# Kernel optimization log

Hardware: AMD Instinct MI355X
Metric: run time of the kernel (lower is better)

## Reference

```python
import jax, jax.numpy as jnp
import numpy as np

B, S, H = 4096, 64, 512


def setup_inputs() -> dict:
    key = jax.random.key(0)
    ks = jax.random.split(key, 10)
    sc = 1.0 / np.sqrt(H)
    return {
        "facts": jax.random.normal(ks[0], (B, S, H), dtype=jnp.float32),
        "G": jax.random.uniform(ks[1], (B, S), dtype=jnp.float32),
        "Wr": jax.random.normal(ks[2], (H, H), dtype=jnp.float32) * sc,
        "br": jnp.zeros((H,), dtype=jnp.float32),
        "Ur": jax.random.normal(ks[3], (H, H), dtype=jnp.float32) * sc,
        "bur": jnp.zeros((H,), dtype=jnp.float32),
        "W": jax.random.normal(ks[4], (H, H), dtype=jnp.float32) * sc,
        "bw": jnp.zeros((H,), dtype=jnp.float32),
        "U": jax.random.normal(ks[5], (H, H), dtype=jnp.float32) * sc,
        "bu": jnp.zeros((H,), dtype=jnp.float32),
    }


def reference(facts, G, Wr, br, Ur, bur, W, bw, U, bu):
    # facts: (B, S, H), G: (B, S) -> output (B, H)
    # Precompute input projections for all steps (batched GEMMs, hoisted out of scan)
    fWr = jnp.einsum('bsh,oh->bso', facts, Wr) + br  # (B,S,H)
    fW = jnp.einsum('bsh,oh->bso', facts, W) + bw    # (B,S,H)

    def step(C, xs):
        fwr_t, fw_t, g_t = xs  # (B,H), (B,H), (B,)
        r = jax.nn.sigmoid(fwr_t + C @ Ur.T + bur)
        h_tilda = jnp.tanh(fw_t + r * (C @ U.T + bu))
        g = g_t[:, None]
        h = g * h_tilda + (1.0 - g) * C
        return h, None

    C0 = jnp.zeros((facts.shape[0], facts.shape[2]), dtype=facts.dtype)
    xs = (jnp.swapaxes(fWr, 0, 1), jnp.swapaxes(fW, 0, 1), G.T)  # time-major
    C, _ = jax.lax.scan(step, C0, xs)
    return C
```

## Files before the change

kernel.cpp:

```cpp
#include <hip/hip_runtime.h>

#define B_ 4096
#define S_ 64
#define H_ 512
#define BM 128
#define BN 64
#define BK 64
#define NIT (H_ / BK)

typedef _Float16 half8 __attribute__((ext_vector_type(8)));
typedef _Float16 half4 __attribute__((ext_vector_type(4)));
typedef float float4v __attribute__((ext_vector_type(4)));
typedef unsigned int uint4v __attribute__((ext_vector_type(4)));

__global__ void convert_weights_kernel(const float* __restrict__ Wr, const float* __restrict__ W,
                                       const float* __restrict__ Ur, const float* __restrict__ U,
                                       _Float16* __restrict__ out) {
    const float* src;
    switch (blockIdx.y) {
        case 0: src = Wr; break;
        case 1: src = W;  break;
        case 2: src = Ur; break;
        default: src = U; break;
    }
    int i = (blockIdx.x * blockDim.x + threadIdx.x) * 8;
    float4v a = *(const float4v*)(src + i);
    float4v b = *(const float4v*)(src + i + 4);
    half8 h;
    h[0] = (_Float16)a[0]; h[1] = (_Float16)a[1]; h[2] = (_Float16)a[2]; h[3] = (_Float16)a[3];
    h[4] = (_Float16)b[0]; h[5] = (_Float16)b[1]; h[6] = (_Float16)b[2]; h[7] = (_Float16)b[3];
    *(half8*)(out + (size_t)blockIdx.y * H_ * H_ + i) = h;
}

template<bool LAST>
__global__ __launch_bounds__(256, 1)
void gru_step_kernel(const float* __restrict__ facts, const float* __restrict__ G,
                     const _Float16* __restrict__ wf,
                     const float* __restrict__ br, const float* __restrict__ bur,
                     const float* __restrict__ bw, const float* __restrict__ bu,
                     const _Float16* __restrict__ c_in, _Float16* __restrict__ c_out,
                     float* __restrict__ out32, int t)
{
    extern __shared__ _Float16 sm[];
    const int tid = threadIdx.x;
    const int lane = tid & 63;
    const int wid = tid >> 6;
    const int l15 = lane & 15;
    const int l4  = lane >> 4;
    const int wm = wid >> 1;
    const int wn = wid & 1;
    const int b0 = blockIdx.x * BM;
    const int n0 = blockIdx.y * BN;

    float4v acc[4][4][2];
#pragma unroll
    for (int w = 0; w < 4; ++w)
#pragma unroll
        for (int m = 0; m < 4; ++m)
#pragma unroll
            for (int n = 0; n < 2; ++n)
                acc[w][m][n] = (float4v){0.f, 0.f, 0.f, 0.f};

    float4v sf[8];
    uint4v  scv[4];
    uint4v  swv[8];

    const int f_row = wid * 32 + l4;
    const int f_col = l15 * 4;
    const int c_row = wid * 32 + (lane >> 3);
    const int c_chk = lane & 7;
    const int w_row = lane >> 3;

    const float* fbase = facts + ((size_t)b0 * S_ + t) * H_;

    auto issue = [&](int kk) {
        const int k0 = kk * BK;
#pragma unroll
        for (int j = 0; j < 8; ++j)
            sf[j] = *(const float4v*)(fbase + (size_t)(f_row + j * 4) * (S_ * H_) + k0 + f_col);
#pragma unroll
        for (int j = 0; j < 4; ++j)
            scv[j] = *(const uint4v*)(c_in + (size_t)(b0 + c_row + j * 8) * H_ + k0 + c_chk * 8);
#pragma unroll
        for (int j = 0; j < 8; ++j)
            swv[j] = *(const uint4v*)(wf + (size_t)wid * (H_ * H_) + (size_t)(n0 + w_row + j * 8) * H_ + k0 + c_chk * 8);
    };

    auto stage = [&](int sel) {
        _Float16* bf  = sm + sel * 32768;
        _Float16* bc  = bf + 8192;
        _Float16* bwt = bf + 16384;
#pragma unroll
        for (int j = 0; j < 8; ++j) {
            int row = f_row + j * 4;
            half4 h;
            h[0] = (_Float16)sf[j][0]; h[1] = (_Float16)sf[j][1];
            h[2] = (_Float16)sf[j][2]; h[3] = (_Float16)sf[j][3];
            int c16 = (l15 >> 1) ^ (row & 7);
            *(half4*)&bf[row * 64 + c16 * 8 + (l15 & 1) * 4] = h;
        }
#pragma unroll
        for (int j = 0; j < 4; ++j) {
            int row = c_row + j * 8;
            *(uint4v*)&bc[row * 64 + ((c_chk ^ (row & 7)) << 3)] = scv[j];
        }
#pragma unroll
        for (int j = 0; j < 8; ++j) {
            int row = w_row + j * 8;
            *(uint4v*)&bwt[(wid * 64 + row) * 64 + ((c_chk ^ (row & 7)) << 3)] = swv[j];
        }
    };

    auto compute = [&](int sel) {
        const _Float16* bf  = sm + sel * 32768;
        const _Float16* bc  = bf + 8192;
        const _Float16* bwt = bf + 16384;
#pragma unroll
        for (int s = 0; s < 2; ++s) {
            half8 fa[4], fc[4], wb[4][2];
            const int kc = s * 4 + l4;
#pragma unroll
            for (int m = 0; m < 4; ++m) {
                int row = wm * 64 + m * 16 + l15;
                int off = row * 64 + ((kc ^ (row & 7)) << 3);
                fa[m] = *(const half8*)&bf[off];
                fc[m] = *(const half8*)&bc[off];
            }
#pragma unroll
            for (int w = 0; w < 4; ++w)
#pragma unroll
                for (int n = 0; n < 2; ++n) {
                    int row = wn * 32 + n * 16 + l15;
                    wb[w][n] = *(const half8*)&bwt[(w * 64 + row) * 64 + ((kc ^ (row & 7)) << 3)];
                }
#pragma unroll
            for (int m = 0; m < 4; ++m)
#pragma unroll
                for (int n = 0; n < 2; ++n) {
                    acc[0][m][n] = __builtin_amdgcn_mfma_f32_16x16x32_f16(fa[m], wb[0][n], acc[0][m][n], 0, 0, 0);
                    acc[1][m][n] = __builtin_amdgcn_mfma_f32_16x16x32_f16(fa[m], wb[1][n], acc[1][m][n], 0, 0, 0);
                    acc[2][m][n] = __builtin_amdgcn_mfma_f32_16x16x32_f16(fc[m], wb[2][n], acc[2][m][n], 0, 0, 0);
                    acc[3][m][n] = __builtin_amdgcn_mfma_f32_16x16x32_f16(fc[m], wb[3][n], acc[3][m][n], 0, 0, 0);
                }
        }
    };

    issue(0);
#pragma unroll
    for (int kk = 0; kk < NIT; ++kk) {
        stage(kk & 1);
        if (kk + 1 < NIT) issue(kk + 1);
        __syncthreads();
        compute(kk & 1);
    }

    const int col_base = n0 + wn * 32;
    const int row_base = b0 + wm * 64;
#pragma unroll
    for (int n = 0; n < 2; ++n) {
        const int col = col_base + n * 16 + l15;
        const float brv = br[col] + bur[col];
        const float bwv = bw[col];
        const float buv = bu[col];
#pragma unroll
        for (int m = 0; m < 4; ++m) {
#pragma unroll
            for (int r = 0; r < 4; ++r) {
                const int row = row_base + m * 16 + l4 * 4 + r;
                float apre = acc[0][m][n][r] + acc[2][m][n][r] + brv;
                float rg = 1.0f / (1.0f + __expf(-apre));
                float x = (acc[1][m][n][r] + bwv) + rg * (acc[3][m][n][r] + buv);
                float e2 = __expf(2.0f * x);
                float ht = 1.0f - 2.0f / (e2 + 1.0f);
                float g = G[(size_t)row * S_ + t];
                float cold = (float)c_in[(size_t)row * H_ + col];
                float h = g * ht + (1.0f - g) * cold;
                if (LAST) out32[(size_t)row * H_ + col] = h;
                else      c_out[(size_t)row * H_ + col] = (_Float16)h;
            }
        }
    }
}

extern "C" void kernel_launch(void* const* d_in, const int* in_sizes, int n_in,
                              void* d_out, int out_size, void* d_ws, size_t ws_size,
                              hipStream_t stream) {
    const float* facts = (const float*)d_in[0];
    const float* G     = (const float*)d_in[1];
    const float* Wr    = (const float*)d_in[2];
    const float* br    = (const float*)d_in[3];
    const float* Ur    = (const float*)d_in[4];
    const float* bur   = (const float*)d_in[5];
    const float* W     = (const float*)d_in[6];
    const float* bw    = (const float*)d_in[7];
    const float* U     = (const float*)d_in[8];
    const float* bu    = (const float*)d_in[9];

    _Float16* wf16 = (_Float16*)d_ws;
    _Float16* c0   = wf16 + 4 * H_ * H_;
    _Float16* c1   = c0 + (size_t)B_ * H_;

    hipMemsetAsync(c0, 0, (size_t)B_ * H_ * sizeof(_Float16), stream);
    convert_weights_kernel<<<dim3(H_ * H_ / (256 * 8), 4), 256, 0, stream>>>(Wr, W, Ur, U, wf16);

    dim3 grid(B_ / BM, H_ / BN);
    const size_t lds = 131072;
    _Float16* bufs[2] = {c0, c1};
    for (int t = 0; t < S_; ++t) {
        _Float16* cin  = bufs[t & 1];
        _Float16* cout = bufs[(t & 1) ^ 1];
        if (t == S_ - 1)
            gru_step_kernel<true><<<grid, 256, lds, stream>>>(facts, G, wf16, br, bur, bw, bu,
                                                              cin, cout, (float*)d_out, t);
        else
            gru_step_kernel<false><<<grid, 256, lds, stream>>>(facts, G, wf16, br, bur, bw, bu,
                                                               cin, cout, nullptr, t);
    }
}
```

Before: 1.922 ms.

## Hoist input projections into one batched GEMM, leaving only recurrent GEMMs per step

Splits the work into a single up-front GEMM that computes facts·[Wr;W]^T plus biases for all time steps into a time-major fp16 buffer P, and a slimmer per-step kernel that only multiplies the hidden state by Ur and U. The per-step kernel reads the precomputed projections from P in its epilogue. The step kernel also uses smaller tiles, less LDS and two blocks per CU for more occupancy. The cost is a large extra fp16 workspace buffer (S·B·1024 halves) plus its write and reread traffic, and an extra rounding of the projections to fp16.

```diff
diff --git a/kernel.cpp b/kernel.cpp
--- a/kernel.cpp
+++ b/kernel.cpp
@@ -3,10 +3,6 @@
 #define B_ 4096
 #define S_ 64
 #define H_ 512
-#define BM 128
-#define BN 64
-#define BK 64
-#define NIT (H_ / BK)
 
 typedef _Float16 half8 __attribute__((ext_vector_type(8)));
 typedef _Float16 half4 __attribute__((ext_vector_type(4)));
@@ -32,14 +28,10 @@
     *(half8*)(out + (size_t)blockIdx.y * H_ * H_ + i) = h;
 }
 
-template<bool LAST>
-__global__ __launch_bounds__(256, 1)
-void gru_step_kernel(const float* __restrict__ facts, const float* __restrict__ G,
-                     const _Float16* __restrict__ wf,
-                     const float* __restrict__ br, const float* __restrict__ bur,
-                     const float* __restrict__ bw, const float* __restrict__ bu,
-                     const _Float16* __restrict__ c_in, _Float16* __restrict__ c_out,
-                     float* __restrict__ out32, int t)
+__global__ __launch_bounds__(256, 2)
+void gemm_p_kernel(const float* __restrict__ facts, const _Float16* __restrict__ wAB,
+                   const float* __restrict__ br, const float* __restrict__ bur,
+                   const float* __restrict__ bw, _Float16* __restrict__ P)
 {
     extern __shared__ _Float16 sm[];
     const int tid = threadIdx.x;
@@ -47,49 +39,38 @@
     const int wid = tid >> 6;
     const int l15 = lane & 15;
     const int l4  = lane >> 4;
-    const int wm = wid >> 1;
-    const int wn = wid & 1;
-    const int b0 = blockIdx.x * BM;
-    const int n0 = blockIdx.y * BN;
-
-    float4v acc[4][4][2];
-#pragma unroll
-    for (int w = 0; w < 4; ++w)
-#pragma unroll
-        for (int m = 0; m < 4; ++m)
-#pragma unroll
-            for (int n = 0; n < 2; ++n)
-                acc[w][m][n] = (float4v){0.f, 0.f, 0.f, 0.f};
+    const int wm = wid >> 1, wn = wid & 1;
+    const int bid = blockIdx.x;
+    const int idx = bid & 63;
+    const int mt = (bid >> 6) * 8 + (idx & 7);
+    const int nt = idx >> 3;
+    const int m0 = mt * 128, n0 = nt * 128;
+
+    float4v acc[4][4];
+#pragma unroll
+    for (int m = 0; m < 4; ++m)
+#pragma unroll
+        for (int n = 0; n < 4; ++n) acc[m][n] = (float4v){0.f, 0.f, 0.f, 0.f};
 
     float4v sf[8];
-    uint4v  scv[4];
-    uint4v  swv[8];
-
+    uint4v  swv[4];
     const int f_row = wid * 32 + l4;
     const int f_col = l15 * 4;
-    const int c_row = wid * 32 + (lane >> 3);
-    const int c_chk = lane & 7;
-    const int w_row = lane >> 3;
-
-    const float* fbase = facts + ((size_t)b0 * S_ + t) * H_;
+    const int b_row = wid * 32 + (lane >> 3);
+    const int b_chk = lane & 7;
 
     auto issue = [&](int kk) {
-        const int k0 = kk * BK;
+        const int k0 = kk * 64;
 #pragma unroll
         for (int j = 0; j < 8; ++j)
-            sf[j] = *(const float4v*)(fbase + (size_t)(f_row + j * 4) * (S_ * H_) + k0 + f_col);
+            sf[j] = *(const float4v*)(facts + (size_t)(m0 + f_row + j * 4) * H_ + k0 + f_col);
 #pragma unroll
         for (int j = 0; j < 4; ++j)
-            scv[j] = *(const uint4v*)(c_in + (size_t)(b0 + c_row + j * 8) * H_ + k0 + c_chk * 8);
-#pragma unroll
-        for (int j = 0; j < 8; ++j)
-            swv[j] = *(const uint4v*)(wf + (size_t)wid * (H_ * H_) + (size_t)(n0 + w_row + j * 8) * H_ + k0 + c_chk * 8);
-    };
-
+            swv[j] = *(const uint4v*)(wAB + (size_t)(n0 + b_row + j * 8) * H_ + k0 + b_chk * 8);
+    };
     auto stage = [&](int sel) {
-        _Float16* bf  = sm + sel * 32768;
-        _Float16* bc  = bf + 8192;
-        _Float16* bwt = bf + 16384;
+        _Float16* bf = sm + sel * 16384;
+        _Float16* bb = bf + 8192;
 #pragma unroll
         for (int j = 0; j < 8; ++j) {
             int row = f_row + j * 4;
@@ -101,83 +82,168 @@
         }
 #pragma unroll
         for (int j = 0; j < 4; ++j) {
+            int row = b_row + j * 8;
+            *(uint4v*)&bb[row * 64 + ((b_chk ^ (row & 7)) << 3)] = swv[j];
+        }
+    };
+    auto compute = [&](int sel) {
+        const _Float16* bf = sm + sel * 16384;
+        const _Float16* bb = bf + 8192;
+#pragma unroll
+        for (int s = 0; s < 2; ++s) {
+            const int kc = s * 4 + l4;
+            half8 fa[4], wb[4];
+#pragma unroll
+            for (int m = 0; m < 4; ++m) {
+                int row = wm * 64 + m * 16 + l15;
+                fa[m] = *(const half8*)&bf[row * 64 + ((kc ^ (row & 7)) << 3)];
+            }
+#pragma unroll
+            for (int n = 0; n < 4; ++n) {
+                int row = wn * 64 + n * 16 + l15;
+                wb[n] = *(const half8*)&bb[row * 64 + ((kc ^ (row & 7)) << 3)];
+            }
+#pragma unroll
+            for (int m = 0; m < 4; ++m)
+#pragma unroll
+                for (int n = 0; n < 4; ++n)
+                    acc[m][n] = __builtin_amdgcn_mfma_f32_16x16x32_f16(fa[m], wb[n], acc[m][n], 0, 0, 0);
+        }
+    };
+
+    issue(0);
+#pragma unroll
+    for (int kk = 0; kk < 8; ++kk) {
+        stage(kk & 1);
+        if (kk + 1 < 8) issue(kk + 1);
+        __syncthreads();
+        compute(kk & 1);
+    }
+
+#pragma unroll
+    for (int n = 0; n < 4; ++n) {
+        const int col = n0 + wn * 64 + n * 16 + l15;
+        const float bias = (col < H_) ? (br[col] + bur[col]) : bw[col - H_];
+#pragma unroll
+        for (int m = 0; m < 4; ++m)
+#pragma unroll
+            for (int r = 0; r < 4; ++r) {
+                int rowl = wm * 64 + m * 16 + l4 * 4 + r;
+                int grow = m0 + rowl;
+                P[((size_t)(rowl & 63) * B_ + (grow >> 6)) * 1024 + col] = (_Float16)(acc[m][n][r] + bias);
+            }
+    }
+}
+
+template<bool LAST>
+__global__ __launch_bounds__(256, 2)
+void gru_step2_kernel(const _Float16* __restrict__ P, const float* __restrict__ G,
+                      const _Float16* __restrict__ wf,
+                      const float* __restrict__ bu,
+                      const _Float16* __restrict__ c_in, _Float16* __restrict__ c_out,
+                      float* __restrict__ out32, int t)
+{
+    extern __shared__ _Float16 sm[];
+    const int tid = threadIdx.x;
+    const int lane = tid & 63;
+    const int wid = tid >> 6;
+    const int l15 = lane & 15;
+    const int l4  = lane >> 4;
+    const int wm = wid >> 1, wn = wid & 1;
+    const int b0 = blockIdx.x * 128;
+    const int n0 = blockIdx.y * 32;
+
+    float4v acc[2][4];
+#pragma unroll
+    for (int f = 0; f < 2; ++f)
+#pragma unroll
+        for (int m = 0; m < 4; ++m) acc[f][m] = (float4v){0.f, 0.f, 0.f, 0.f};
+
+    uint4v scv[4], swv2[2];
+    const int c_row = wid * 32 + (lane >> 3);
+    const int c_chk = lane & 7;
+
+    auto issue = [&](int kk) {
+        const int k0 = kk * 64;
+#pragma unroll
+        for (int j = 0; j < 4; ++j)
+            scv[j] = *(const uint4v*)(c_in + (size_t)(b0 + c_row + j * 8) * H_ + k0 + c_chk * 8);
+#pragma unroll
+        for (int jj = 0; jj < 2; ++jj) {
+            int q = tid * 2 + jj;
+            int fam = q >> 8, row = (q >> 3) & 31, chk = q & 7;
+            swv2[jj] = *(const uint4v*)(wf + (size_t)(2 + fam) * H_ * H_ + (size_t)(n0 + row) * H_ + k0 + chk * 8);
+        }
+    };
+    auto stage = [&](int sel) {
+        _Float16* bc  = sm + sel * 12288;
+        _Float16* bwt = bc + 8192;
+#pragma unroll
+        for (int j = 0; j < 4; ++j) {
             int row = c_row + j * 8;
             *(uint4v*)&bc[row * 64 + ((c_chk ^ (row & 7)) << 3)] = scv[j];
         }
 #pragma unroll
-        for (int j = 0; j < 8; ++j) {
-            int row = w_row + j * 8;
-            *(uint4v*)&bwt[(wid * 64 + row) * 64 + ((c_chk ^ (row & 7)) << 3)] = swv[j];
-        }
-    };
-
+        for (int jj = 0; jj < 2; ++jj) {
+            int q = tid * 2 + jj;
+            int fam = q >> 8, row = (q >> 3) & 31, chk = q & 7;
+            *(uint4v*)&bwt[(fam * 32 + row) * 64 + ((chk ^ (row & 7)) << 3)] = swv2[jj];
+        }
+    };
     auto compute = [&](int sel) {
-        const _Float16* bf  = sm + sel * 32768;
-        const _Float16* bc  = bf + 8192;
-        const _Float16* bwt = bf + 16384;
+        const _Float16* bc  = sm + sel * 12288;
+        const _Float16* bwt = bc + 8192;
 #pragma unroll
         for (int s = 0; s < 2; ++s) {
-            half8 fa[4], fc[4], wb[4][2];
             const int kc = s * 4 + l4;
+            half8 fc[4], wfr[2];
 #pragma unroll
             for (int m = 0; m < 4; ++m) {
                 int row = wm * 64 + m * 16 + l15;
-                int off = row * 64 + ((kc ^ (row & 7)) << 3);
-                fa[m] = *(const half8*)&bf[off];
-                fc[m] = *(const half8*)&bc[off];
-            }
-#pragma unroll
-            for (int w = 0; w < 4; ++w)
-#pragma unroll
-                for (int n = 0; n < 2; ++n) {
-                    int row = wn * 32 + n * 16 + l15;
-                    wb[w][n] = *(const half8*)&bwt[(w * 64 + row) * 64 + ((kc ^ (row & 7)) << 3)];
-                }
-#pragma unroll
-            for (int m = 0; m < 4; ++m)
-#pragma unroll
-                for (int n = 0; n < 2; ++n) {
-                    acc[0][m][n] = __builtin_amdgcn_mfma_f32_16x16x32_f16(fa[m], wb[0][n], acc[0][m][n], 0, 0, 0);
-                    acc[1][m][n] = __builtin_amdgcn_mfma_f32_16x16x32_f16(fa[m], wb[1][n], acc[1][m][n], 0, 0, 0);
-                    acc[2][m][n] = __builtin_amdgcn_mfma_f32_16x16x32_f16(fc[m], wb[2][n], acc[2][m][n], 0, 0, 0);
-                    acc[3][m][n] = __builtin_amdgcn_mfma_f32_16x16x32_f16(fc[m], wb[3][n], acc[3][m][n], 0, 0, 0);
-                }
+                fc[m] = *(const half8*)&bc[row * 64 + ((kc ^ (row & 7)) << 3)];
+            }
+#pragma unroll
+            for (int f = 0; f < 2; ++f) {
+                int row = wn * 16 + l15;
+                wfr[f] = *(const half8*)&bwt[(f * 32 + row) * 64 + ((kc ^ (row & 7)) << 3)];
+            }
+#pragma unroll
+            for (int m = 0; m < 4; ++m) {
+                acc[0][m] = __builtin_amdgcn_mfma_f32_16x16x32_f16(fc[m], wfr[0], acc[0][m], 0, 0, 0);
+                acc[1][m] = __builtin_amdgcn_mfma_f32_16x16x32_f16(fc[m], wfr[1], acc[1][m], 0, 0, 0);
+            }
         }
     };
 
     issue(0);
 #pragma unroll
-    for (int kk = 0; kk < NIT; ++kk) {
+    for (int kk = 0; kk < 8; ++kk) {
         stage(kk & 1);
-        if (kk + 1 < NIT) issue(kk + 1);
+        if (kk + 1 < 8) issue(kk + 1);
         __syncthreads();
         compute(kk & 1);
     }
 
-    const int col_base = n0 + wn * 32;
-    const int row_base = b0 + wm * 64;
-#pragma unroll
-    for (int n = 0; n < 2; ++n) {
-        const int col = col_base + n * 16 + l15;
-        const float brv = br[col] + bur[col];
-        const float bwv = bw[col];
-        const float buv = bu[col];
-#pragma unroll
-        for (int m = 0; m < 4; ++m) {
-#pragma unroll
-            for (int r = 0; r < 4; ++r) {
-                const int row = row_base + m * 16 + l4 * 4 + r;
-                float apre = acc[0][m][n][r] + acc[2][m][n][r] + brv;
-                float rg = 1.0f / (1.0f + __expf(-apre));
-                float x = (acc[1][m][n][r] + bwv) + rg * (acc[3][m][n][r] + buv);
-                float e2 = __expf(2.0f * x);
-                float ht = 1.0f - 2.0f / (e2 + 1.0f);
-                float g = G[(size_t)row * S_ + t];
-                float cold = (float)c_in[(size_t)row * H_ + col];
-                float h = g * ht + (1.0f - g) * cold;
-                if (LAST) out32[(size_t)row * H_ + col] = h;
-                else      c_out[(size_t)row * H_ + col] = (_Float16)h;
-            }
+    const int col = n0 + wn * 16 + l15;
+    const float buv = bu[col];
+    const _Float16* Pt = P + (size_t)t * B_ * 1024;
+#pragma unroll
+    for (int m = 0; m < 4; ++m) {
+#pragma unroll
+        for (int r = 0; r < 4; ++r) {
+            const int row = b0 + wm * 64 + m * 16 + l4 * 4 + r;
+            float p1 = (float)Pt[(size_t)row * 1024 + col];
+            float p2 = (float)Pt[(size_t)row * 1024 + 512 + col];
+            float apre = p1 + acc[0][m][r];
+            float rg = 1.0f / (1.0f + __expf(-apre));
+            float x = p2 + rg * (acc[1][m][r] + buv);
+            float e2 = __expf(2.0f * x);
+            float ht = 1.0f - 2.0f / (e2 + 1.0f);
+            float g = G[(size_t)row * S_ + t];
+            float cold = (float)c_in[(size_t)row * H_ + col];
+            float h = g * ht + (1.0f - g) * cold;
+            if (LAST) out32[(size_t)row * H_ + col] = h;
+            else      c_out[(size_t)row * H_ + col] = (_Float16)h;
         }
     }
 }
@@ -199,21 +265,21 @@
     _Float16* wf16 = (_Float16*)d_ws;
     _Float16* c0   = wf16 + 4 * H_ * H_;
     _Float16* c1   = c0 + (size_t)B_ * H_;
+    _Float16* P    = c1 + (size_t)B_ * H_;
 
     hipMemsetAsync(c0, 0, (size_t)B_ * H_ * sizeof(_Float16), stream);
     convert_weights_kernel<<<dim3(H_ * H_ / (256 * 8), 4), 256, 0, stream>>>(Wr, W, Ur, U, wf16);
 
-    dim3 grid(B_ / BM, H_ / BN);
-    const size_t lds = 131072;
+    gemm_p_kernel<<<16384, 256, 65536, stream>>>(facts, wf16, br, bur, bw, P);
+
+    dim3 grid2(B_ / 128, H_ / 32);
     _Float16* bufs[2] = {c0, c1};
     for (int t = 0; t < S_; ++t) {
         _Float16* cin  = bufs[t & 1];
         _Float16* cout = bufs[(t & 1) ^ 1];
         if (t == S_ - 1)
-            gru_step_kernel<true><<<grid, 256, lds, stream>>>(facts, G, wf16, br, bur, bw, bu,
-                                                              cin, cout, (float*)d_out, t);
+            gru_step2_kernel<true><<<grid2, 256, 49152, stream>>>(P, G, wf16, bu, cin, cout, (float*)d_out, t);
         else
-            gru_step_kernel<false><<<grid, 256, lds, stream>>>(facts, G, wf16, br, bur, bw, bu,
-                                                               cin, cout, nullptr, t);
-    }
-}
+            gru_step2_kernel<false><<<grid2, 256, 49152, stream>>>(P, G, wf16, bu, cin, cout, nullptr, t);
+    }
+}
```

Result: no change. 1.947 ms (+1.3%).
